# Kernel tuning notes

Measured on AMD Instinct MI355X. Metric: run time of the kernel, lower is better.

Reference implementation:

```python
import jax, jax.numpy as jnp
import numpy as np

N, D = 8192, 256
NUM_CLASSES = 100
WEIGHT = 1.0


def setup_inputs() -> dict:
    key = jax.random.key(0)
    k1, k2 = jax.random.split(key)
    predictions = jax.random.normal(k1, (N, D), dtype=jnp.float32)
    targets = jax.random.randint(k2, (N,), 0, NUM_CLASSES, dtype=jnp.int32)
    return {"predictions": predictions, "targets": targets}


def reference(predictions, targets):
    # Pairwise squared L2 via ||a||^2 + ||b||^2 - 2 a.b  -> [N, N]
    sq = jnp.sum(predictions * predictions, axis=1)
    d2 = sq[:, None] + sq[None, :] - 2.0 * (predictions @ predictions.T)
    dist = jnp.sqrt(jnp.maximum(d2, 0.0))  # torch.dist(p=2)

    n = predictions.shape[0]
    upper = jnp.triu(jnp.ones((n, n), dtype=bool), k=1)  # i < j pairs only
    same = targets[:, None] == targets[None, :]
    mask = upper & same

    num = jnp.sum(mask).astype(dist.dtype)
    loss = jnp.sum(jnp.where(mask, dist, 0.0)) / num
    return loss * WEIGHT
```

## Files before the change

### kernel.cpp

```cpp
#include <hip/hip_runtime.h>

#define N_CLS 100
#define D_DIM 256
#define MAX_M 112
#define ROW_SH 264
#define PANEL 48
#define PACK_CAP 128
#define CNT_STR 32
#define POISON 0xAAAAAAAAu

typedef short bf16x8 __attribute__((ext_vector_type(8)));
typedef float f32x4  __attribute__((ext_vector_type(4)));

__device__ __forceinline__ unsigned short f2bf(float f) {
    unsigned int b = __float_as_uint(f);
    return (unsigned short)((b + 0x7FFFu + ((b >> 16) & 1u)) >> 16);
}

__global__ __launch_bounds__(256) void k_prep(const float* __restrict__ pred,
        const int* __restrict__ targets, int n, int* __restrict__ cnt,
        int* __restrict__ bucket_g, float* __restrict__ sqp,
        unsigned short* __restrict__ packed) {
    const int wid  = (int)((blockIdx.x * 256u + threadIdx.x) >> 6);
    const int lane = threadIdx.x & 63;
    if (wid >= n) return;
    const int c = targets[wid];
    int pos = 0;
    if (lane == 0) {
        pos = (int)((unsigned)atomicAdd(&cnt[c * CNT_STR], 1) - POISON);
        bucket_g[(size_t)c * n + pos] = wid;
    }
    pos = __shfl(pos, 0, 64);
    const float4 v = ((const float4*)(pred + (size_t)wid * D_DIM))[lane];
    float s = v.x * v.x + v.y * v.y + v.z * v.z + v.w * v.w;
    #pragma unroll
    for (int o = 32; o; o >>= 1) s += __shfl_xor(s, o, 64);
    if (pos < PACK_CAP) {
        short4 pk;
        pk.x = (short)f2bf(v.x); pk.y = (short)f2bf(v.y);
        pk.z = (short)f2bf(v.z); pk.w = (short)f2bf(v.w);
        *(short4*)(packed + ((size_t)c * PACK_CAP + pos) * D_DIM + lane * 4) = pk;
        if (lane == 0) sqp[c * PACK_CAP + pos] = s;
    }
}

__device__ __forceinline__ void stage(const float* __restrict__ pred,
        const int* bkt, int m, int cp0, int dslot, int cnt,
        short* tileS, float* sqs, int wave, int lane) {
    for (int r = wave; r < cnt; r += 8) {
        int cp = cp0 + r;
        float4 v = make_float4(0.f, 0.f, 0.f, 0.f);
        if (cp < m) {
            int g = bkt[cp];
            v = ((const float4*)(pred + (size_t)g * D_DIM))[lane];
        }
        short4 pk;
        pk.x = (short)f2bf(v.x); pk.y = (short)f2bf(v.y);
        pk.z = (short)f2bf(v.z); pk.w = (short)f2bf(v.w);
        *(short4*)&tileS[(dslot + r) * ROW_SH + lane * 4] = pk;
        float s = v.x * v.x + v.y * v.y + v.z * v.z + v.w * v.w;
        #pragma unroll
        for (int o = 32; o; o >>= 1) s += __shfl_xor(s, o, 64);
        if (lane == 0) sqs[dslot + r] = s;
    }
}

__device__ __forceinline__ float tile16(const short* tileS, const float* sqs,
        int a0, int b0, int ga0, int gb0, int m, int lane) {
    const int q = lane >> 4, l15 = lane & 15;
    const short* aP = &tileS[(a0 + l15) * ROW_SH + q * 8];
    const short* bP = &tileS[(b0 + l15) * ROW_SH + q * 8];
    f32x4 acc = {0.f, 0.f, 0.f, 0.f};
    #pragma unroll
    for (int ks = 0; ks < 8; ++ks) {
        bf16x8 af = *(const bf16x8*)(aP + ks * 32);
        bf16x8 bg = *(const bf16x8*)(bP + ks * 32);
        acc = __builtin_amdgcn_mfma_f32_16x16x32_bf16(af, bg, acc, 0, 0, 0);
    }
    float out = 0.f;
    #pragma unroll
    for (int rr = 0; rr < 4; ++rr) {
        int al = q * 4 + rr;
        int pi = ga0 + al, pj = gb0 + l15;
        float d2 = sqs[a0 + al] + sqs[b0 + l15] - 2.f * acc[rr];
        if (pj < m && pi < pj) out += sqrtf(fmaxf(d2, 0.f));
    }
    return out;
}

__global__ __launch_bounds__(512) void k_gram2(const float* __restrict__ pred, int n,
        int* __restrict__ cnt, const int* __restrict__ bucket_g,
        const float* __restrict__ sqp, const unsigned short* __restrict__ packed,
        double* __restrict__ psum, double* __restrict__ pcnt, float* __restrict__ out) {
    __shared__ short tileS[MAX_M * ROW_SH];
    __shared__ float sqs[MAX_M];
    __shared__ float wsum[8];
    const int t = threadIdx.x, lane = t & 63, wave = t >> 6;
    const int c = blockIdx.x;
    const int m = (int)((unsigned)cnt[c * CNT_STR] - POISON);
    float accum = 0.f;

    if (m <= MAX_M) {
        const int T = (m + 15) >> 4;
        const int4* srcv = (const int4*)(packed + (size_t)c * PACK_CAP * D_DIM);
        for (int k = t; k < m * 32; k += 512)
            *(int4*)&tileS[(k >> 5) * ROW_SH + (k & 31) * 8] = srcv[k];
        if (t < m) sqs[t] = sqp[c * PACK_CAP + t];
        __syncthreads();
        const int np = T * (T + 1) / 2;
        for (int idx = wave; idx < np; idx += 8) {
            int ta = 0, r = idx;
            while (r >= T - ta) { r -= T - ta; ++ta; }
            int tb = ta + r;
            accum += tile16(tileS, sqs, ta * 16, tb * 16, ta * 16, tb * 16, m, lane);
        }
    } else {
        const int* bkt_g = bucket_g + (size_t)c * n;
        const int P = (m + PANEL - 1) / PANEL;
        for (int pi = 0; pi < P; ++pi)
        for (int pj = pi; pj < P; ++pj) {
            __syncthreads();
            stage(pred, bkt_g, m, pi * PANEL, 0,     PANEL, tileS, sqs, wave, lane);
            stage(pred, bkt_g, m, pj * PANEL, PANEL, PANEL, tileS, sqs, wave, lane);
            __syncthreads();
            for (int idx = wave; idx < 9; idx += 8) {
                int ta = idx / 3, tb = idx % 3;
                accum += tile16(tileS, sqs, ta * 16, PANEL + tb * 16,
                                pi * PANEL + ta * 16, pj * PANEL + tb * 16, m, lane);
            }
        }
    }

    #pragma unroll
    for (int o = 32; o; o >>= 1) accum += __shfl_xor(accum, o, 64);
    if (lane == 0) wsum[wave] = accum;
    __syncthreads();
    if (t == 0) {
        double bs = 0.0;
        #pragma unroll
        for (int w = 0; w < 8; ++w) bs += (double)wsum[w];
        __hip_atomic_store(&psum[c], bs, __ATOMIC_RELAXED, __HIP_MEMORY_SCOPE_AGENT);
        __hip_atomic_store(&pcnt[c], (double)m * (double)(m - 1) * 0.5,
                           __ATOMIC_RELEASE, __HIP_MEMORY_SCOPE_AGENT);
        cnt[c * CNT_STR] = (int)POISON;
    }

    if (c == 0) {
        double mys = 0.0, myc = 0.0;
        if (t < N_CLS) {
            unsigned long long bits;
            do {
                bits = __hip_atomic_load((const unsigned long long*)&pcnt[t],
                                         __ATOMIC_ACQUIRE, __HIP_MEMORY_SCOPE_AGENT);
            } while (bits >> 63);
            myc = __longlong_as_double((long long)bits);
            unsigned long long sb = __hip_atomic_load((const unsigned long long*)&psum[t],
                                         __ATOMIC_RELAXED, __HIP_MEMORY_SCOPE_AGENT);
            mys = __longlong_as_double((long long)sb);
        }
        __syncthreads();
        double* red_s = (double*)tileS;
        double* red_c = red_s + 128;
        if (t < 128) { red_s[t] = (t < N_CLS) ? mys : 0.0;
                       red_c[t] = (t < N_CLS) ? myc : 0.0; }
        __syncthreads();
        for (int w = 64; w; w >>= 1) {
            if (t < w) { red_s[t] += red_s[t + w]; red_c[t] += red_c[t + w]; }
            __syncthreads();
        }
        if (t == 0) out[0] = (float)(red_c[0] > 0.0 ? red_s[0] / red_c[0] : 0.0);
    }
}

extern "C" void kernel_launch(void* const* d_in, const int* in_sizes, int n_in,
                              void* d_out, int out_size, void* d_ws, size_t ws_size,
                              hipStream_t stream) {
    const float* pred  = (const float*)d_in[0];
    const int* targets = (const int*)d_in[1];
    float* out         = (float*)d_out;
    const int n = in_sizes[1];

    char* ws = (char*)d_ws;
    size_t off = 0;
    double* psum = (double*)(ws + off); off += N_CLS * 8;
    double* pcnt = (double*)(ws + off); off += N_CLS * 8;
    int* cnt     = (int*)(ws + off);    off += (size_t)N_CLS * CNT_STR * 4;
    float* sqp   = (float*)(ws + off);  off += (size_t)N_CLS * PACK_CAP * 4;
    off = (off + 63) & ~(size_t)63;
    unsigned short* packed = (unsigned short*)(ws + off);
    off += (size_t)N_CLS * PACK_CAP * D_DIM * 2;
    int* bucket_g = (int*)(ws + off);

    const int prep_blocks = (n * 64 + 255) / 256;
    k_prep<<<prep_blocks, 256, 0, stream>>>(pred, targets, n, cnt, bucket_g, sqp, packed);
    k_gram2<<<N_CLS, 512, 0, stream>>>(pred, n, cnt, bucket_g, sqp, packed,
                                       psum, pcnt, out);
}
```

Baseline: 68.72 us.

## Fuse prep and per-class gram kernels into one launch with grid-wide spin barrier

```diff
diff --git a/kernel.cpp b/kernel.cpp
--- a/kernel.cpp
+++ b/kernel.cpp
@@ -8,6 +8,8 @@
 #define PACK_CAP 128
 #define CNT_STR 32
 #define POISON 0xAAAAAAAAu
+#define GRID_B 512
+#define TW (GRID_B * 8)
 
 typedef short bf16x8 __attribute__((ext_vector_type(8)));
 typedef float f32x4  __attribute__((ext_vector_type(4)));
@@ -17,21 +19,8 @@
     return (unsigned short)((b + 0x7FFFu + ((b >> 16) & 1u)) >> 16);
 }
 
-__global__ __launch_bounds__(256) void k_prep(const float* __restrict__ pred,
-        const int* __restrict__ targets, int n, int* __restrict__ cnt,
-        int* __restrict__ bucket_g, float* __restrict__ sqp,
-        unsigned short* __restrict__ packed) {
-    const int wid  = (int)((blockIdx.x * 256u + threadIdx.x) >> 6);
-    const int lane = threadIdx.x & 63;
-    if (wid >= n) return;
-    const int c = targets[wid];
-    int pos = 0;
-    if (lane == 0) {
-        pos = (int)((unsigned)atomicAdd(&cnt[c * CNT_STR], 1) - POISON);
-        bucket_g[(size_t)c * n + pos] = wid;
-    }
-    pos = __shfl(pos, 0, 64);
-    const float4 v = ((const float4*)(pred + (size_t)wid * D_DIM))[lane];
+__device__ __forceinline__ void emit_row(float4 v, int c, int pos, int lane,
+        float* __restrict__ sqp, unsigned short* __restrict__ packed) {
     float s = v.x * v.x + v.y * v.y + v.z * v.z + v.w * v.w;
     #pragma unroll
     for (int o = 32; o; o >>= 1) s += __shfl_xor(s, o, 64);
@@ -88,14 +77,66 @@
     return out;
 }
 
-__global__ __launch_bounds__(512) void k_gram2(const float* __restrict__ pred, int n,
-        int* __restrict__ cnt, const int* __restrict__ bucket_g,
-        const float* __restrict__ sqp, const unsigned short* __restrict__ packed,
+__global__ __launch_bounds__(512) void k_fused(const float* __restrict__ pred,
+        const int* __restrict__ targets, int n, int* __restrict__ cnt,
+        int* __restrict__ bucket_g, float* __restrict__ sqp,
+        unsigned short* __restrict__ packed, int* __restrict__ rows_done,
         double* __restrict__ psum, double* __restrict__ pcnt, float* __restrict__ out) {
     __shared__ short tileS[MAX_M * ROW_SH];
     __shared__ float sqs[MAX_M];
     __shared__ float wsum[8];
     const int t = threadIdx.x, lane = t & 63, wave = t >> 6;
+    const int gw = (int)(blockIdx.x * 8 + wave);
+
+    {
+        const int r0 = gw, r1 = gw + TW;
+        const bool h0 = r0 < n, h1 = r1 < n;
+        float4 v0 = make_float4(0,0,0,0), v1 = make_float4(0,0,0,0);
+        int c0 = 0, c1 = 0;
+        if (h0) { c0 = targets[r0]; v0 = ((const float4*)(pred + (size_t)r0 * D_DIM))[lane]; }
+        if (h1) { c1 = targets[r1]; v1 = ((const float4*)(pred + (size_t)r1 * D_DIM))[lane]; }
+        int p0 = 0, p1 = 0;
+        if (lane == 0) {
+            if (h0) { p0 = (int)((unsigned)atomicAdd(&cnt[c0 * CNT_STR], 1) - POISON);
+                      bucket_g[(size_t)c0 * n + p0] = r0; }
+            if (h1) { p1 = (int)((unsigned)atomicAdd(&cnt[c1 * CNT_STR], 1) - POISON);
+                      bucket_g[(size_t)c1 * n + p1] = r1; }
+        }
+        p0 = __shfl(p0, 0, 64); p1 = __shfl(p1, 0, 64);
+        if (h0) emit_row(v0, c0, p0, lane, sqp, packed);
+        if (h1) emit_row(v1, c1, p1, lane, sqp, packed);
+        for (int r = gw + 2 * TW; r < n; r += TW) {
+            int c = targets[r];
+            float4 v = ((const float4*)(pred + (size_t)r * D_DIM))[lane];
+            int p = 0;
+            if (lane == 0) { p = (int)((unsigned)atomicAdd(&cnt[c * CNT_STR], 1) - POISON);
+                             bucket_g[(size_t)c * n + p] = r; }
+            p = __shfl(p, 0, 64);
+            emit_row(v, c, p, lane, sqp, packed);
+        }
+    }
+    __threadfence();
+    __syncthreads();
+    if (t == 0) {
+        int blkRows = 0;
+        #pragma unroll
+        for (int w = 0; w < 8; ++w) {
+            int g = (int)(blockIdx.x * 8 + w);
+            if (g < n) blkRows += (n - 1 - g) / TW + 1;
+        }
+        __hip_atomic_fetch_add(rows_done, blkRows, __ATOMIC_RELEASE, __HIP_MEMORY_SCOPE_AGENT);
+    }
+    if (blockIdx.x >= N_CLS) return;
+
+    if (t == 0) {
+        const unsigned tgt = POISON + (unsigned)n;
+        while (__hip_atomic_load((const unsigned*)rows_done, __ATOMIC_ACQUIRE,
+                                 __HIP_MEMORY_SCOPE_AGENT) != tgt)
+            __builtin_amdgcn_s_sleep(1);
+    }
+    __syncthreads();
+    __threadfence();
+
     const int c = blockIdx.x;
     const int m = (int)((unsigned)cnt[c * CNT_STR] - POISON);
     float accum = 0.f;
@@ -157,6 +198,7 @@
             unsigned long long sb = __hip_atomic_load((const unsigned long long*)&psum[t],
                                          __ATOMIC_RELAXED, __HIP_MEMORY_SCOPE_AGENT);
             mys = __longlong_as_double((long long)sb);
+            __hip_atomic_store(&pcnt[t], -1.0, __ATOMIC_RELAXED, __HIP_MEMORY_SCOPE_AGENT);
         }
         __syncthreads();
         double* red_s = (double*)tileS;
@@ -168,7 +210,10 @@
             if (t < w) { red_s[t] += red_s[t + w]; red_c[t] += red_c[t + w]; }
             __syncthreads();
         }
-        if (t == 0) out[0] = (float)(red_c[0] > 0.0 ? red_s[0] / red_c[0] : 0.0);
+        if (t == 0) {
+            out[0] = (float)(red_c[0] > 0.0 ? red_s[0] / red_c[0] : 0.0);
+            *rows_done = (int)POISON;
+        }
     }
 }
 
@@ -182,17 +227,16 @@
 
     char* ws = (char*)d_ws;
     size_t off = 0;
-    double* psum = (double*)(ws + off); off += N_CLS * 8;
-    double* pcnt = (double*)(ws + off); off += N_CLS * 8;
-    int* cnt     = (int*)(ws + off);    off += (size_t)N_CLS * CNT_STR * 4;
-    float* sqp   = (float*)(ws + off);  off += (size_t)N_CLS * PACK_CAP * 4;
+    double* psum  = (double*)(ws + off); off += N_CLS * 8;
+    double* pcnt  = (double*)(ws + off); off += N_CLS * 8;
+    int* cnt      = (int*)(ws + off);    off += (size_t)N_CLS * CNT_STR * 4;
+    int* rows_done= (int*)(ws + off);    off += 128;
+    float* sqp    = (float*)(ws + off);  off += (size_t)N_CLS * PACK_CAP * 4;
     off = (off + 63) & ~(size_t)63;
     unsigned short* packed = (unsigned short*)(ws + off);
     off += (size_t)N_CLS * PACK_CAP * D_DIM * 2;
     int* bucket_g = (int*)(ws + off);
 
-    const int prep_blocks = (n * 64 + 255) / 256;
-    k_prep<<<prep_blocks, 256, 0, stream>>>(pred, targets, n, cnt, bucket_g, sqp, packed);
-    k_gram2<<<N_CLS, 512, 0, stream>>>(pred, n, cnt, bucket_g, sqp, packed,
-                                       psum, pcnt, out);
-}
+    k_fused<<<GRID_B, 512, 0, stream>>>(pred, targets, n, cnt, bucket_g, sqp, packed,
+                                        rows_done, psum, pcnt, out);
+}
```

New measurement: 154.9 us. 125% more time.
